# Kernel tuning notes

Measured on AMD Instinct MI355X. Metric: run time of the kernel, lower is better.

## Reference

```python
import jax, jax.numpy as jnp
import numpy as np

DIM = 512
N_HEADS = 8
HEAD_DIM = DIM // N_HEADS
BN_EPS = 1e-5


def setup_inputs() -> dict:
    key = jax.random.key(0)
    ks = jax.random.split(key, 8)
    B, C, H, W = 16, DIM, 32, 32
    x = jax.random.normal(ks[0], (B, C, H, W), dtype=jnp.float32)
    # 1x1 convs == channel matmuls: stacked q/k/v weights [3, out, in], proj [out, in]
    w_qkv = jax.random.normal(ks[1], (3, DIM, DIM), dtype=jnp.float32) * (DIM ** -0.5)
    w_proj = jax.random.normal(ks[2], (DIM, DIM), dtype=jnp.float32) * (DIM ** -0.5)
    # BatchNorm (inference form) params for q/k/v branches, stacked [3, C]
    bn_gamma = jax.random.uniform(ks[3], (3, DIM), minval=0.5, maxval=1.5)
    bn_beta = jax.random.normal(ks[4], (3, DIM)) * 0.1
    bn_mean = jax.random.normal(ks[5], (3, DIM)) * 0.1
    bn_var = jax.random.uniform(ks[6], (3, DIM), minval=0.5, maxval=1.5)
    return {"x": x, "w_qkv": w_qkv, "w_proj": w_proj, "bn_gamma": bn_gamma,
            "bn_beta": bn_beta, "bn_mean": bn_mean, "bn_var": bn_var}


def _ternary_ste(t):
    # forward: sign(t) in {-1,0,1}; backward: identity (straight-through)
    return t + jax.lax.stop_gradient(jnp.sign(t) - t)


def reference(x, w_qkv, w_proj, bn_gamma, bn_beta, bn_mean, bn_var):
    B, C, H, W = x.shape
    N = H * W
    xf = x.reshape(B, C, N)
    # fused 1x1 conv for q,k,v: [3,B,C,N]
    qkv = jnp.einsum('koc,bcn->kbon', w_qkv, xf)
    # BatchNorm (inference): y = (x - mean)/sqrt(var+eps)*gamma + beta
    s = bn_gamma / jnp.sqrt(bn_var + BN_EPS)          # [3,C]
    b = bn_beta - bn_mean * s                          # [3,C]
    qkv = qkv * s[:, None, :, None] + b[:, None, :, None]
    q = _ternary_ste(qkv[0]).reshape(B, N_HEADS, HEAD_DIM, N)
    k = _ternary_ste(qkv[1]).reshape(B, N_HEADS, HEAD_DIM, N)
    v = qkv[2].reshape(B, N_HEADS, HEAD_DIM, N)
    scale = HEAD_DIM ** -0.5
    attn = jnp.einsum('bhdn,bhen->bhde', q, k) * scale  # [B,h,d,d] channel-wise attn
    attn = jax.nn.softmax(attn, axis=-1)
    out = jnp.einsum('bhde,bhen->bhdn', attn, v).reshape(B, C, N)
    out = jnp.einsum('oc,bcn->bon', w_proj, out) + xf   # proj + residual
    return out.reshape(B, C, H, W)
```

## Files before the change

### kernel.cpp

```cpp
#include <hip/hip_runtime.h>
#include <math.h>

#define BN_EPS 1e-5f
#define FIXC 1.0e-4f

typedef _Float16 f16;
typedef _Float16 f16x4 __attribute__((ext_vector_type(4)));
typedef _Float16 f16x8 __attribute__((ext_vector_type(8)));
typedef float f32x4 __attribute__((ext_vector_type(4)));
typedef int i32x4 __attribute__((ext_vector_type(4)));

static constexpr int BB = 16;
static constexpr int C  = 512;
static constexpr int NP = 1024;
static constexpr int NH = 8;
static constexpr int HD = 64;
static constexpr int M3 = 1536;


static constexpr size_t OFF_WHI  = 0;
static constexpr size_t OFF_WLO  = 1572864;
static constexpr size_t OFF_WPH  = 3145728;
static constexpr size_t OFF_SB   = 3670016;
static constexpr size_t OFF_WN   = 3682304;
static constexpr size_t OFF_XN   = 3686400;
static constexpr size_t OFF_FLAG = 3751936;
static constexpr size_t OFF_XTH  = 5849088;
static constexpr size_t OFF_XTL  = 22626304;
static constexpr size_t OFF_AOT  = OFF_XTH;
static constexpr size_t OFF_Q    = 39403520;
static constexpr size_t OFF_K    = 47792128;
static constexpr size_t OFF_VT   = 56180736;

__device__ __forceinline__ void gld16(const void* g, void* l) {
  __builtin_amdgcn_global_load_lds(
      (const __attribute__((address_space(1))) void*)g,
      (__attribute__((address_space(3))) void*)l, 16, 0, 0);
}

__device__ __forceinline__ size_t frag_off(int tile, int kt, int row7, int k5) {
  return (((size_t)tile * 16 + kt) * 8 + (row7 >> 4)) * 512
       + (size_t)((row7 & 15) | ((k5 >> 3) << 4)) * 8;
}

__global__ __launch_bounds__(256) void k_convW(
    const float* __restrict__ wqkv, const float* __restrict__ wproj,
    const float* __restrict__ g, const float* __restrict__ be,
    const float* __restrict__ mu, const float* __restrict__ va,
    f16* __restrict__ Whi, f16* __restrict__ Wlo, f16* __restrict__ Wph,
    float* __restrict__ sA, float* __restrict__ bA)
{
  const int i = blockIdx.x * 256 + threadIdx.x;
  {
    const int m = i >> 6, l = i & 63;
    const float4 v0 = *(const float4*)&wqkv[(size_t)m * C + l * 8];
    const float4 v1 = *(const float4*)&wqkv[(size_t)m * C + l * 8 + 4];
    const float vv[8] = {v0.x, v0.y, v0.z, v0.w, v1.x, v1.y, v1.z, v1.w};
    f16x8 hv, lv;
#pragma unroll
    for (int q = 0; q < 8; ++q) {
      const f16 h = (f16)vv[q];
      hv[q] = h; lv[q] = (f16)(vv[q] - (float)h);
    }
    *(f16x8*)&Whi[frag_off(m >> 7, l >> 2, m & 127, (l & 3) * 8)] = hv;
    *(f16x8*)&Wlo[(size_t)m * C + l * 8] = lv;
  }
  if (i < 32768) {
    const int m = i >> 6, l = i & 63;
    const float4 v0 = *(const float4*)&wproj[(size_t)m * C + l * 8];
    const float4 v1 = *(const float4*)&wproj[(size_t)m * C + l * 8 + 4];
    const float vv[8] = {v0.x, v0.y, v0.z, v0.w, v1.x, v1.y, v1.z, v1.w};
    f16x8 hv;
#pragma unroll
    for (int q = 0; q < 8; ++q) hv[q] = (f16)vv[q];
    *(f16x8*)&Wph[frag_off(m >> 7, l >> 2, m & 127, (l & 3) * 8)] = hv;
  }
  if (i < M3) {
    const float s = g[i] / sqrtf(va[i] + BN_EPS);
    sA[i] = s;
    bA[i] = be[i] - mu[i] * s;
  }
}

__global__ __launch_bounds__(256) void k_wnorm(
    const float* __restrict__ wqkv, float* __restrict__ wnorm)
{
  const int row = blockIdx.x * 4 + (threadIdx.x >> 6);
  const int lane = threadIdx.x & 63;
  const float4 v0 = *(const float4*)&wqkv[(size_t)row * C + lane * 8];
  const float4 v1 = *(const float4*)&wqkv[(size_t)row * C + lane * 8 + 4];
  float s = v0.x * v0.x + v0.y * v0.y + v0.z * v0.z + v0.w * v0.w
          + v1.x * v1.x + v1.y * v1.y + v1.z * v1.z + v1.w * v1.w;
  s += __shfl_xor(s, 1);  s += __shfl_xor(s, 2);  s += __shfl_xor(s, 4);
  s += __shfl_xor(s, 8);  s += __shfl_xor(s, 16); s += __shfl_xor(s, 32);
  if (lane == 0) wnorm[row] = sqrtf(s);
}

__global__ __launch_bounds__(256) void k_convX(
    const float* __restrict__ x, f16* __restrict__ XtH, f16* __restrict__ XtL,
    float* __restrict__ xnorm2)
{
  const int k0 = blockIdx.x * 64, n0 = blockIdx.y * 64, b = blockIdx.z;
  __shared__ float ls[64][65];
  const int t = threadIdx.x;
  const float* xp = x + ((size_t)b * C + k0) * NP + n0;
  const int c4 = (t & 15) * 4, r0 = t >> 4;
#pragma unroll
  for (int q = 0; q < 4; ++q) {
    const float4 v = *(const float4*)(xp + (size_t)(r0 + q * 16) * NP + c4);
    ls[r0 + q * 16][c4 + 0] = v.x; ls[r0 + q * 16][c4 + 1] = v.y;
    ls[r0 + q * 16][c4 + 2] = v.z; ls[r0 + q * 16][c4 + 3] = v.w;
  }
  __syncthreads();
  if (t < 64) {
    float s2 = 0.f;
#pragma unroll
    for (int q = 0; q < 64; ++q) { const float v = ls[q][t]; s2 = fmaf(v, v, s2); }
    atomicAdd(&xnorm2[(b << 10) + n0 + t], s2);
  }
  const int n = t >> 2, kk = (t & 3) * 16;
  const int n_abs = n0 + n;
  f16x8 hv0 = {}, hv1 = {}, lv0 = {}, lv1 = {};
#pragma unroll
  for (int q = 0; q < 8; ++q) {
    const float v = ls[kk + q][n];
    const f16 h = (f16)v;
    hv0[q] = h; lv0[q] = (f16)(v - (float)h);
  }
#pragma unroll
  for (int q = 0; q < 8; ++q) {
    const float v = ls[kk + 8 + q][n];
    const f16 h = (f16)v;
    hv1[q] = h; lv1[q] = (f16)(v - (float)h);
  }
  const int kb0 = k0 + kk, kb1 = k0 + kk + 8;
  *(f16x8*)&XtH[frag_off(b * 8 + (n_abs >> 7), kb0 >> 5, n_abs & 127, kb0 & 31)] = hv0;
  *(f16x8*)&XtH[frag_off(b * 8 + (n_abs >> 7), kb1 >> 5, n_abs & 127, kb1 & 31)] = hv1;
  *(f16x8*)&XtL[((size_t)b * NP + n_abs) * C + kb0] = lv0;
  *(f16x8*)&XtL[((size_t)b * NP + n_abs) * C + kb1] = lv1;
}

__global__ __launch_bounds__(256) void k_qkv_mfma(
    const f16* __restrict__ Whi, const f16* __restrict__ XtH,
    const float* __restrict__ sA, const float* __restrict__ bA,
    const float* __restrict__ wnorm, const float* __restrict__ xnorm2,
    signed char* __restrict__ qw, signed char* __restrict__ kw,
    f16* __restrict__ vt, unsigned* __restrict__ flagbits)
{
  __shared__ __align__(16) f16 SMEM[32768];
  f16* const As0 = SMEM;
  f16* const Bs0 = SMEM + 8192;
  f16* const As1 = SMEM + 16384;
  f16* const Bs1 = SMEM + 24576;

  const int t = threadIdx.x, lane = t & 63, wid = t >> 6;
  const int n0 = blockIdx.x * 128, m0 = blockIdx.y * 128, b = blockIdx.z;

  const f16* Af = Whi + (size_t)(m0 >> 7) * 65536;
  const f16* Bf = XtH + ((size_t)b * 8 + (n0 >> 7)) * 65536;

  f32x4 acc[4][4];
#pragma unroll
  for (int i = 0; i < 4; ++i)
#pragma unroll
    for (int j = 0; j < 4; ++j) acc[i][j] = (f32x4){0.f, 0.f, 0.f, 0.f};

  const int wm = wid >> 1, wn = wid & 1;
  const int lr = lane & 15, ls = lane >> 4;
  const int soff = wid * 512 + lane * 8;

#define QSTAGE(TI, AS, BS) do {                                         \
    const f16* Ak_ = Af + (size_t)(TI) * 8192;                          \
    const f16* Bk_ = Bf + (size_t)(TI) * 8192;                          \
    _Pragma("unroll")                                                   \
    for (int r_ = 0; r_ < 4; ++r_) {                                    \
      gld16(Ak_ + r_ * 2048 + soff, &(AS)[r_ * 2048 + wid * 512]);      \
      gld16(Bk_ + r_ * 2048 + soff, &(BS)[r_ * 2048 + wid * 512]);      \
    }                                                                   \
  } while (0)

#define QCOMP(AS, BS) do {                                              \
    _Pragma("unroll")                                                   \
    for (int ksub_ = 0; ksub_ < 2; ++ksub_) {                           \
      f16x8 ah_[4], bh_[4];                                             \
      _Pragma("unroll")                                                 \
      for (int i_ = 0; i_ < 4; ++i_) {                                  \
        ah_[i_] = *(const f16x8*)&(AS)[ksub_ * 4096 + (wm * 4 + i_) * 512 + lane * 8]; \
        bh_[i_] = *(const f16x8*)&(BS)[ksub_ * 4096 + (wn * 4 + i_) * 512 + lane * 8]; \
      }                                                                 \
      _Pragma("unroll")                                                 \
      for (int i_ = 0; i_ < 4; ++i_)                                    \
        _Pragma("unroll")                                               \
        for (int j_ = 0; j_ < 4; ++j_)                                  \
          acc[i_][j_] = __builtin_amdgcn_mfma_f32_16x16x32_f16(         \
              ah_[i_], bh_[j_], acc[i_][j_], 0, 0, 0);                  \
    }                                                                   \
  } while (0)

  QSTAGE(0, As0, Bs0);
#pragma unroll
  for (int ti = 0; ti < 8; ++ti) {
    if (ti < 7) {
      if (ti & 1) QSTAGE(ti + 1, As0, Bs0);
      else        QSTAGE(ti + 1, As1, Bs1);
      asm volatile("s_waitcnt vmcnt(8)" ::: "memory");
    } else {
      asm volatile("s_waitcnt vmcnt(0)" ::: "memory");
    }
    __builtin_amdgcn_sched_barrier(0);
    __builtin_amdgcn_s_barrier();
    if (ti & 1) QCOMP(As1, Bs1); else QCOMP(As0, Bs0);
    asm volatile("s_waitcnt lgkmcnt(0)" ::: "memory");
    __builtin_amdgcn_sched_barrier(0);
    __builtin_amdgcn_s_barrier();
  }

#undef QSTAGE
#undef QCOMP

  const int kidx = m0 >> 9;
  if (kidx != 2) {
    signed char* dst0 = (kidx == 0) ? qw : kw;
    float xnrm[4];
#pragma unroll
    for (int j = 0; j < 4; ++j)
      xnrm[j] = sqrtf(xnorm2[(b << 10) + n0 + wn * 64 + j * 16 + lr]);
#pragma unroll
    for (int i = 0; i < 4; ++i) {
      float sv[4], bv[4], dl[4];
#pragma unroll
      for (int r = 0; r < 4; ++r) {
        const int o = m0 + wm * 64 + i * 16 + ls * 4 + r;
        sv[r] = sA[o]; bv[r] = bA[o];
        dl[r] = FIXC * wnorm[o] * sv[r];
      }
      const int oc0 = (m0 & 511) + wm * 64 + i * 16 + ls * 4;
      const int og0 = m0 + wm * 64 + i * 16 + ls * 4;
#pragma unroll
      for (int j = 0; j < 4; ++j) {
        const int n = n0 + wn * 64 + j * 16 + lr;
#pragma unroll
        for (int r = 0; r < 4; ++r) {
          const float z = fmaf(acc[i][j][r], sv[r], bv[r]);
          dst0[((size_t)b * C + oc0 + r) * NP + n] =
              (signed char)((z > 0.f) - (z < 0.f));
          if (fabsf(z) <= dl[r] * xnrm[j]) {
            const int of = og0 + r;
            atomicOr(&flagbits[(((size_t)b * NP + n) << 5) + (of >> 5)],
                     1u << (of & 31));
          }
        }
      }
    }
  } else {
    const int c0 = m0 & 511;
    for (int hf = 0; hf < 2; ++hf) {
      __syncthreads();
      if (wn == hf) {
#pragma unroll
        for (int i = 0; i < 4; ++i) {
          float sv[4], bv[4];
#pragma unroll
          for (int r = 0; r < 4; ++r) {
            const int o = m0 + wm * 64 + i * 16 + ls * 4 + r;
            sv[r] = sA[o]; bv[r] = bA[o];
          }
#pragma unroll
          for (int j = 0; j < 4; ++j) {
            f16x4 pk;
#pragma unroll
            for (int r = 0; r < 4; ++r)
              pk[r] = (f16)fmaf(acc[i][j][r], sv[r], bv[r]);
            *(f16x4*)&SMEM[(size_t)(j * 16 + lr) * 136 + wm * 64 + i * 16 + ls * 4] = pk;
          }
        }
      }
      __syncthreads();
      const int nl = t >> 2, cc = (t & 3) * 32;
      const f16* src = &SMEM[(size_t)nl * 136 + cc];
      f16x8 r0 = *(const f16x8*)(src + 0);
      f16x8 r1 = *(const f16x8*)(src + 8);
      f16x8 r2 = *(const f16x8*)(src + 16);
      f16x8 r3 = *(const f16x8*)(src + 24);
      f16* dstv = vt + ((size_t)b * NP + n0 + hf * 64 + nl) * C + c0 + cc;
      *(f16x8*)(dstv + 0)  = r0;
      *(f16x8*)(dstv + 8)  = r1;
      *(f16x8*)(dstv + 16) = r2;
      *(f16x8*)(dstv + 24) = r3;
    }
  }
}

__global__ __launch_bounds__(256) void k_fix(
    const unsigned* __restrict__ flagbits,
    const f16* __restrict__ Whi, const f16* __restrict__ Wlo,
    const f16* __restrict__ XtH, const f16* __restrict__ XtL,
    const float* __restrict__ sA, const float* __restrict__ bA,
    signed char* __restrict__ qw, signed char* __restrict__ kw)
{
  const int wv = blockIdx.x * 4 + (threadIdx.x >> 6);
  const int lane = threadIdx.x & 63;
  const int b = wv >> 10, n = wv & 1023;

  const unsigned* bm = flagbits + ((size_t)wv << 5);
  const unsigned myw = (lane < 32) ? bm[lane] : 0u;
  if (__ballot(myw != 0) == 0ULL) return;

  const int kb = lane * 8;
  const f16x8 bhv = *(const f16x8*)&XtH[
      frag_off(b * 8 + (n >> 7), kb >> 5, n & 127, kb & 31)];
  const f16x8 blv = *(const f16x8*)&XtL[((size_t)b * NP + n) * C + kb];
  float xv[8];
#pragma unroll
  for (int q = 0; q < 8; ++q) xv[q] = (float)bhv[q] + (float)blv[q];

  for (int w = 0; w < 32; ++w) {
    unsigned bits = __shfl(myw, w);
    while (bits) {
      const int o = w * 32 + __builtin_ctz(bits);
      bits &= bits - 1;
      const f16x8 ahv = *(const f16x8*)&Whi[
          frag_off(o >> 7, kb >> 5, o & 127, kb & 31)];
      const f16x8 alv = *(const f16x8*)&Wlo[(size_t)o * C + kb];
      float s = 0.f;
#pragma unroll
      for (int q = 0; q < 8; ++q)
        s = fmaf((float)ahv[q] + (float)alv[q], xv[q], s);
      s += __shfl_xor(s, 1);  s += __shfl_xor(s, 2);  s += __shfl_xor(s, 4);
      s += __shfl_xor(s, 8);  s += __shfl_xor(s, 16); s += __shfl_xor(s, 32);
      if (lane == 0) {
        const float y = fmaf(s, sA[o], bA[o]);
        const signed char sg = (signed char)((y > 0.f) - (y < 0.f));
        if (o < 512) qw[((size_t)b * C + o) * NP + n] = sg;
        else         kw[((size_t)b * C + (o - 512)) * NP + n] = sg;
      }
    }
  }
}

__global__ __launch_bounds__(256) void k_attn_fused(
    const signed char* __restrict__ qw, const signed char* __restrict__ kw,
    const f16* __restrict__ vt, f16* __restrict__ aot)
{
  const int half = blockIdx.x;
  const int bh = blockIdx.y;
  const int b = bh >> 3, h = bh & 7;
  const int t = threadIdx.x, lane = t & 63, wid = t >> 6;
  const int dw = wid * 16;
  const int lr = lane & 15, lg = lane >> 4;

  __shared__ f16 ph[64][72];
  __shared__ f16 pl[64][72];
  __shared__ f16 sb[64][72];

  const signed char* qp = qw + ((size_t)b * C + h * HD + dw + lr) * NP;
  const signed char* kp = kw + ((size_t)b * C + h * HD + lr) * NP;

  i32x4 accS[4];
#pragma unroll
  for (int j = 0; j < 4; ++j) accS[j] = (i32x4){0, 0, 0, 0};

#pragma unroll 4
  for (int ks = 0; ks < 16; ++ks) {
    const i32x4 af = *(const i32x4*)(qp + ks * 64 + lg * 16);
#pragma unroll
    for (int j = 0; j < 4; ++j) {
      const i32x4 bf = *(const i32x4*)(kp + (size_t)(j * 16) * NP + ks * 64 + lg * 16);
      accS[j] = __builtin_amdgcn_mfma_i32_16x16x64_i8(af, bf, accS[j], 0, 0, 0);
    }
  }

#pragma unroll
  for (int r = 0; r < 4; ++r) {
    float mx = (float)accS[0][r];
#pragma unroll
    for (int j = 1; j < 4; ++j) mx = fmaxf(mx, (float)accS[j][r]);
    mx = fmaxf(mx, __shfl_xor(mx, 1));
    mx = fmaxf(mx, __shfl_xor(mx, 2));
    mx = fmaxf(mx, __shfl_xor(mx, 4));
    mx = fmaxf(mx, __shfl_xor(mx, 8));
    float pvv[4];
    float sm = 0.f;
#pragma unroll
    for (int j = 0; j < 4; ++j) {
      pvv[j] = expf(((float)accS[j][r] - mx) * 0.125f);
      sm += pvv[j];
    }
    sm += __shfl_xor(sm, 1);
    sm += __shfl_xor(sm, 2);
    sm += __shfl_xor(sm, 4);
    sm += __shfl_xor(sm, 8);
    const float inv = 1.f / sm;
    const int drow = dw + lg * 4 + r;
#pragma unroll
    for (int j = 0; j < 4; ++j) {
      const float p = pvv[j] * inv;
      const f16 hi = (f16)p;
      ph[drow][j * 16 + lr] = hi;
      pl[drow][j * 16 + lr] = (f16)(p - (float)hi);
    }
  }
  __syncthreads();

  const f16x8 pa0h = *(const f16x8*)&ph[dw + lr][lg * 8];
  const f16x8 pa0l = *(const f16x8*)&pl[dw + lr][lg * 8];
  const f16x8 pa1h = *(const f16x8*)&ph[dw + lr][32 + lg * 8];
  const f16x8 pa1l = *(const f16x8*)&pl[dw + lr][32 + lg * 8];

  const f16* vbase = vt + (size_t)b * NP * C + h * HD;
  const int nbase = half * 512;

  for (int nc = 0; nc < 8; ++nc) {
    const int nn0 = nbase + nc * 64;
    __syncthreads();
#pragma unroll
    for (int nt = 0; nt < 4; ++nt) {
      const f16* vp = vbase + (size_t)(nn0 + nt * 16 + lr) * C + lg * 8;
      const f16x8 bv0 = *(const f16x8*)(vp);
      const f16x8 bv1 = *(const f16x8*)(vp + 32);
      f32x4 acc = (f32x4){0.f, 0.f, 0.f, 0.f};
      acc = __builtin_amdgcn_mfma_f32_16x16x32_f16(pa0h, bv0, acc, 0, 0, 0);
      acc = __builtin_amdgcn_mfma_f32_16x16x32_f16(pa0l, bv0, acc, 0, 0, 0);
      acc = __builtin_amdgcn_mfma_f32_16x16x32_f16(pa1h, bv1, acc, 0, 0, 0);
      acc = __builtin_amdgcn_mfma_f32_16x16x32_f16(pa1l, bv1, acc, 0, 0, 0);
      f16x4 pk;
#pragma unroll
      for (int r = 0; r < 4; ++r) pk[r] = (f16)acc[r];
      *(f16x4*)&sb[nt * 16 + lr][dw + lg * 4] = pk;
    }
    __syncthreads();
    const int nl = t >> 2, cc = (t & 3) * 16;
    const f16x8 o0 = *(const f16x8*)&sb[nl][cc];
    const f16x8 o1 = *(const f16x8*)&sb[nl][cc + 8];
    const int n_abs = nn0 + nl;
    const int c1 = h * HD + cc, c2 = h * HD + cc + 8;
    *(f16x8*)&aot[frag_off(b * 8 + (n_abs >> 7), c1 >> 5, n_abs & 127, c1 & 31)] = o0;
    *(f16x8*)&aot[frag_off(b * 8 + (n_abs >> 7), c2 >> 5, n_abs & 127, c2 & 31)] = o1;
  }
}

__global__ __launch_bounds__(256) void k_proj_mfma(
    const f16* __restrict__ Wph, const f16* __restrict__ aot,
    const float* __restrict__ X, float* __restrict__ out)
{
  __shared__ __align__(16) f16 SMEM[32768];
  f16* const As0 = SMEM;
  f16* const Bs0 = SMEM + 8192;
  f16* const As1 = SMEM + 16384;
  f16* const Bs1 = SMEM + 24576;

  const int t = threadIdx.x, lane = t & 63, wid = t >> 6;
  const int n0 = blockIdx.x * 128, m0 = blockIdx.y * 128, b = blockIdx.z;

  const f16* Af = Wph + (size_t)(m0 >> 7) * 65536;
  const f16* Bf = aot + ((size_t)b * 8 + (n0 >> 7)) * 65536;

  f32x4 acc[4][4];
#pragma unroll
  for (int i = 0; i < 4; ++i)
#pragma unroll
    for (int j = 0; j < 4; ++j) acc[i][j] = (f32x4){0.f, 0.f, 0.f, 0.f};

  const int wm = wid >> 1, wn = wid & 1;
  const int lr = lane & 15, ls = lane >> 4;
  const int soff = wid * 512 + lane * 8;

#define PSTAGE(TI, AS, BS) do {                                         \
    const f16* Ak_ = Af + (size_t)(TI) * 8192;                          \
    const f16* Bk_ = Bf + (size_t)(TI) * 8192;                          \
    _Pragma("unroll")                                                   \
    for (int r_ = 0; r_ < 4; ++r_) {                                    \
      gld16(Ak_ + r_ * 2048 + soff, &(AS)[r_ * 2048 + wid * 512]);      \
      gld16(Bk_ + r_ * 2048 + soff, &(BS)[r_ * 2048 + wid * 512]);      \
    }                                                                   \
  } while (0)

#define PCOMP(AS, BS) do {                                              \
    _Pragma("unroll")                                                   \
    for (int ksub_ = 0; ksub_ < 2; ++ksub_) {                           \
      f16x8 ah_[4], bh_[4];                                             \
      _Pragma("unroll")                                                 \
      for (int i_ = 0; i_ < 4; ++i_) {                                  \
        ah_[i_] = *(const f16x8*)&(AS)[ksub_ * 4096 + (wm * 4 + i_) * 512 + lane * 8]; \
        bh_[i_] = *(const f16x8*)&(BS)[ksub_ * 4096 + (wn * 4 + i_) * 512 + lane * 8]; \
      }                                                                 \
      _Pragma("unroll")                                                 \
      for (int i_ = 0; i_ < 4; ++i_)                                    \
        _Pragma("unroll")                                               \
        for (int j_ = 0; j_ < 4; ++j_)                                  \
          acc[i_][j_] = __builtin_amdgcn_mfma_f32_16x16x32_f16(         \
              ah_[i_], bh_[j_], acc[i_][j_], 0, 0, 0);                  \
    }                                                                   \
  } while (0)

  PSTAGE(0, As0, Bs0);
#pragma unroll
  for (int ti = 0; ti < 8; ++ti) {
    if (ti < 7) {
      if (ti & 1) PSTAGE(ti + 1, As0, Bs0);
      else        PSTAGE(ti + 1, As1, Bs1);
      asm volatile("s_waitcnt vmcnt(8)" ::: "memory");
    } else {
      asm volatile("s_waitcnt vmcnt(0)" ::: "memory");
    }
    __builtin_amdgcn_sched_barrier(0);
    __builtin_amdgcn_s_barrier();
    if (ti & 1) PCOMP(As1, Bs1); else PCOMP(As0, Bs0);
    asm volatile("s_waitcnt lgkmcnt(0)" ::: "memory");
    __builtin_amdgcn_sched_barrier(0);
    __builtin_amdgcn_s_barrier();
  }

#undef PSTAGE
#undef PCOMP

#pragma unroll
  for (int i = 0; i < 4; ++i) {
    const int oc0 = m0 + wm * 64 + i * 16 + ls * 4;
#pragma unroll
    for (int j = 0; j < 4; ++j) {
      const int n = n0 + wn * 64 + j * 16 + lr;
#pragma unroll
      for (int r = 0; r < 4; ++r) {
        const size_t idx = ((size_t)b * C + oc0 + r) * NP + n;
        out[idx] = acc[i][j][r] + X[idx];
      }
    }
  }
}

extern "C" void kernel_launch(void* const* d_in, const int* in_sizes, int n_in,
                              void* d_out, int out_size, void* d_ws, size_t ws_size,
                              hipStream_t stream)
{
  const float* x      = (const float*)d_in[0];
  const float* w_qkv  = (const float*)d_in[1];
  const float* w_proj = (const float*)d_in[2];
  const float* g      = (const float*)d_in[3];
  const float* be     = (const float*)d_in[4];
  const float* mu     = (const float*)d_in[5];
  const float* va     = (const float*)d_in[6];
  float* out = (float*)d_out;

  char* ws = (char*)d_ws;
  f16*  Whi = (f16*)(ws + OFF_WHI);
  f16*  Wlo = (f16*)(ws + OFF_WLO);
  f16*  Wph = (f16*)(ws + OFF_WPH);
  float* sA = (float*)(ws + OFF_SB);
  float* bA = sA + M3;
  float* wn = (float*)(ws + OFF_WN);
  float* xn2 = (float*)(ws + OFF_XN);
  unsigned* flagbits = (unsigned*)(ws + OFF_FLAG);
  f16*  XtH = (f16*)(ws + OFF_XTH);
  f16*  XtL = (f16*)(ws + OFF_XTL);
  f16*  aot = (f16*)(ws + OFF_AOT);
  signed char* qw = (signed char*)(ws + OFF_Q);
  signed char* kw = (signed char*)(ws + OFF_K);
  f16*  vtw = (f16*)(ws + OFF_VT);

  hipMemsetAsync(xn2, 0, OFF_XTH - OFF_XN, stream);

  k_convW<<<dim3(384), 256, 0, stream>>>(
      w_qkv, w_proj, g, be, mu, va, Whi, Wlo, Wph, sA, bA);
  k_wnorm<<<dim3(256), 256, 0, stream>>>(w_qkv, wn);
  k_convX<<<dim3(C / 64, NP / 64, BB), 256, 0, stream>>>(x, XtH, XtL, xn2);
  k_qkv_mfma<<<dim3(NP / 128, M3 / 128, BB), 256, 0, stream>>>(
      Whi, XtH, sA, bA, wn, xn2, qw, kw, vtw, flagbits);
  k_fix<<<dim3(BB * NP / 4), 256, 0, stream>>>(
      flagbits, Whi, Wlo, XtH, XtL, sA, bA, qw, kw);
  k_attn_fused<<<dim3(2, BB * NH), 256, 0, stream>>>(qw, kw, vtw, aot);
  k_proj_mfma<<<dim3(NP / 128, C / 128, BB), 256, 0, stream>>>(Wph, aot, x, out);
}
```

Measured before the change: 136.7 us.

## Fuse wnorm into convW, load QKV fragments directly to registers, split attention quarters

The separate weight-norm kernel is folded into k_convW via a wave shuffle reduction, which removes one launch. The QKV MFMA kernel drops its LDS double-buffered staging and barriers. Each wave now loads pre-fragmented operands straight from global memory into registers with a three-deep software pipeline, and shared memory shrinks so two blocks per CU can fit. The attention kernel is split into four N-chunks instead of two, doubling grid parallelism at the cost of recomputing the QK softmax in more blocks. The risk is that register-direct global loads lose the cross-wave reuse that LDS provided, since the A and B fragments are now read by two waves each.

```diff
diff --git a/kernel.cpp b/kernel.cpp
--- a/kernel.cpp
+++ b/kernel.cpp
@@ -48,7 +48,7 @@
     const float* __restrict__ g, const float* __restrict__ be,
     const float* __restrict__ mu, const float* __restrict__ va,
     f16* __restrict__ Whi, f16* __restrict__ Wlo, f16* __restrict__ Wph,
-    float* __restrict__ sA, float* __restrict__ bA)
+    float* __restrict__ sA, float* __restrict__ bA, float* __restrict__ wnorm)
 {
   const int i = blockIdx.x * 256 + threadIdx.x;
   {
@@ -57,13 +57,21 @@
     const float4 v1 = *(const float4*)&wqkv[(size_t)m * C + l * 8 + 4];
     const float vv[8] = {v0.x, v0.y, v0.z, v0.w, v1.x, v1.y, v1.z, v1.w};
     f16x8 hv, lv;
+    float s2 = 0.f;
 #pragma unroll
     for (int q = 0; q < 8; ++q) {
       const f16 h = (f16)vv[q];
       hv[q] = h; lv[q] = (f16)(vv[q] - (float)h);
+      s2 = fmaf(vv[q], vv[q], s2);
     }
     *(f16x8*)&Whi[frag_off(m >> 7, l >> 2, m & 127, (l & 3) * 8)] = hv;
     *(f16x8*)&Wlo[(size_t)m * C + l * 8] = lv;
+    if (m < 1024) {
+      s2 += __shfl_xor(s2, 1);  s2 += __shfl_xor(s2, 2);
+      s2 += __shfl_xor(s2, 4);  s2 += __shfl_xor(s2, 8);
+      s2 += __shfl_xor(s2, 16); s2 += __shfl_xor(s2, 32);
+      if (l == 0) wnorm[m] = sqrtf(s2);
+    }
   }
   if (i < 32768) {
     const int m = i >> 6, l = i & 63;
@@ -82,20 +90,6 @@
   }
 }
 
-__global__ __launch_bounds__(256) void k_wnorm(
-    const float* __restrict__ wqkv, float* __restrict__ wnorm)
-{
-  const int row = blockIdx.x * 4 + (threadIdx.x >> 6);
-  const int lane = threadIdx.x & 63;
-  const float4 v0 = *(const float4*)&wqkv[(size_t)row * C + lane * 8];
-  const float4 v1 = *(const float4*)&wqkv[(size_t)row * C + lane * 8 + 4];
-  float s = v0.x * v0.x + v0.y * v0.y + v0.z * v0.z + v0.w * v0.w
-          + v1.x * v1.x + v1.y * v1.y + v1.z * v1.z + v1.w * v1.w;
-  s += __shfl_xor(s, 1);  s += __shfl_xor(s, 2);  s += __shfl_xor(s, 4);
-  s += __shfl_xor(s, 8);  s += __shfl_xor(s, 16); s += __shfl_xor(s, 32);
-  if (lane == 0) wnorm[row] = sqrtf(s);
-}
-
 __global__ __launch_bounds__(256) void k_convX(
     const float* __restrict__ x, f16* __restrict__ XtH, f16* __restrict__ XtL,
     float* __restrict__ xnorm2)
@@ -140,18 +134,14 @@
   *(f16x8*)&XtL[((size_t)b * NP + n_abs) * C + kb1] = lv1;
 }
 
-__global__ __launch_bounds__(256) void k_qkv_mfma(
+__global__ __launch_bounds__(256, 2) void k_qkv_mfma(
     const f16* __restrict__ Whi, const f16* __restrict__ XtH,
     const float* __restrict__ sA, const float* __restrict__ bA,
     const float* __restrict__ wnorm, const float* __restrict__ xnorm2,
     signed char* __restrict__ qw, signed char* __restrict__ kw,
     f16* __restrict__ vt, unsigned* __restrict__ flagbits)
 {
-  __shared__ __align__(16) f16 SMEM[32768];
-  f16* const As0 = SMEM;
-  f16* const Bs0 = SMEM + 8192;
-  f16* const As1 = SMEM + 16384;
-  f16* const Bs1 = SMEM + 24576;
+  __shared__ __align__(16) f16 SMEM[8704];
 
   const int t = threadIdx.x, lane = t & 63, wid = t >> 6;
   const int n0 = blockIdx.x * 128, m0 = blockIdx.y * 128, b = blockIdx.z;
@@ -167,56 +157,47 @@
 
   const int wm = wid >> 1, wn = wid & 1;
   const int lr = lane & 15, ls = lane >> 4;
-  const int soff = wid * 512 + lane * 8;
-
-#define QSTAGE(TI, AS, BS) do {                                         \
-    const f16* Ak_ = Af + (size_t)(TI) * 8192;                          \
-    const f16* Bk_ = Bf + (size_t)(TI) * 8192;                          \
+
+#define LOADF(KT, AR, BR) do {                                          \
     _Pragma("unroll")                                                   \
-    for (int r_ = 0; r_ < 4; ++r_) {                                    \
-      gld16(Ak_ + r_ * 2048 + soff, &(AS)[r_ * 2048 + wid * 512]);      \
-      gld16(Bk_ + r_ * 2048 + soff, &(BS)[r_ * 2048 + wid * 512]);      \
+    for (int i_ = 0; i_ < 4; ++i_) {                                    \
+      (AR)[i_] = *(const f16x8*)&Af[(size_t)(KT) * 4096 + (wm * 4 + i_) * 512 + lane * 8]; \
+      (BR)[i_] = *(const f16x8*)&Bf[(size_t)(KT) * 4096 + (wn * 4 + i_) * 512 + lane * 8]; \
     }                                                                   \
   } while (0)
 
-#define QCOMP(AS, BS) do {                                              \
+#define COMPF(AR, BR) do {                                              \
     _Pragma("unroll")                                                   \
-    for (int ksub_ = 0; ksub_ < 2; ++ksub_) {                           \
-      f16x8 ah_[4], bh_[4];                                             \
+    for (int i_ = 0; i_ < 4; ++i_)                                      \
       _Pragma("unroll")                                                 \
-      for (int i_ = 0; i_ < 4; ++i_) {                                  \
-        ah_[i_] = *(const f16x8*)&(AS)[ksub_ * 4096 + (wm * 4 + i_) * 512 + lane * 8]; \
-        bh_[i_] = *(const f16x8*)&(BS)[ksub_ * 4096 + (wn * 4 + i_) * 512 + lane * 8]; \
-      }                                                                 \
-      _Pragma("unroll")                                                 \
-      for (int i_ = 0; i_ < 4; ++i_)                                    \
-        _Pragma("unroll")                                               \
-        for (int j_ = 0; j_ < 4; ++j_)                                  \
-          acc[i_][j_] = __builtin_amdgcn_mfma_f32_16x16x32_f16(         \
-              ah_[i_], bh_[j_], acc[i_][j_], 0, 0, 0);                  \
-    }                                                                   \
+      for (int j_ = 0; j_ < 4; ++j_)                                    \
+        acc[i_][j_] = __builtin_amdgcn_mfma_f32_16x16x32_f16(           \
+            (AR)[i_], (BR)[j_], acc[i_][j_], 0, 0, 0);                  \
   } while (0)
 
-  QSTAGE(0, As0, Bs0);
-#pragma unroll
-  for (int ti = 0; ti < 8; ++ti) {
-    if (ti < 7) {
-      if (ti & 1) QSTAGE(ti + 1, As0, Bs0);
-      else        QSTAGE(ti + 1, As1, Bs1);
-      asm volatile("s_waitcnt vmcnt(8)" ::: "memory");
-    } else {
-      asm volatile("s_waitcnt vmcnt(0)" ::: "memory");
-    }
-    __builtin_amdgcn_sched_barrier(0);
-    __builtin_amdgcn_s_barrier();
-    if (ti & 1) QCOMP(As1, Bs1); else QCOMP(As0, Bs0);
-    asm volatile("s_waitcnt lgkmcnt(0)" ::: "memory");
-    __builtin_amdgcn_sched_barrier(0);
-    __builtin_amdgcn_s_barrier();
-  }
-
-#undef QSTAGE
-#undef QCOMP
+  {
+    f16x8 a0[4], b0[4], a1[4], b1[4], a2[4], b2[4];
+    LOADF(0, a0, b0); LOADF(1, a1, b1);
+    LOADF(2,  a2, b2); COMPF(a0, b0);
+    LOADF(3,  a0, b0); COMPF(a1, b1);
+    LOADF(4,  a1, b1); COMPF(a2, b2);
+    LOADF(5,  a2, b2); COMPF(a0, b0);
+    LOADF(6,  a0, b0); COMPF(a1, b1);
+    LOADF(7,  a1, b1); COMPF(a2, b2);
+    LOADF(8,  a2, b2); COMPF(a0, b0);
+    LOADF(9,  a0, b0); COMPF(a1, b1);
+    LOADF(10, a1, b1); COMPF(a2, b2);
+    LOADF(11, a2, b2); COMPF(a0, b0);
+    LOADF(12, a0, b0); COMPF(a1, b1);
+    LOADF(13, a1, b1); COMPF(a2, b2);
+    LOADF(14, a2, b2); COMPF(a0, b0);
+    LOADF(15, a0, b0); COMPF(a1, b1);
+    COMPF(a2, b2);
+    COMPF(a0, b0);
+  }
+
+#undef LOADF
+#undef COMPF
 
   const int kidx = m0 >> 9;
   if (kidx != 2) {
@@ -342,7 +323,7 @@
     const signed char* __restrict__ qw, const signed char* __restrict__ kw,
     const f16* __restrict__ vt, f16* __restrict__ aot)
 {
-  const int half = blockIdx.x;
+  const int quarter = blockIdx.x;
   const int bh = blockIdx.y;
   const int b = bh >> 3, h = bh & 7;
   const int t = threadIdx.x, lane = t & 63, wid = t >> 6;
@@ -408,9 +389,9 @@
   const f16x8 pa1l = *(const f16x8*)&pl[dw + lr][32 + lg * 8];
 
   const f16* vbase = vt + (size_t)b * NP * C + h * HD;
-  const int nbase = half * 512;
-
-  for (int nc = 0; nc < 8; ++nc) {
+  const int nbase = quarter * 256;
+
+  for (int nc = 0; nc < 4; ++nc) {
     const int nn0 = nbase + nc * 64;
     __syncthreads();
 #pragma unroll
@@ -561,13 +542,12 @@
   hipMemsetAsync(xn2, 0, OFF_XTH - OFF_XN, stream);
 
   k_convW<<<dim3(384), 256, 0, stream>>>(
-      w_qkv, w_proj, g, be, mu, va, Whi, Wlo, Wph, sA, bA);
-  k_wnorm<<<dim3(256), 256, 0, stream>>>(w_qkv, wn);
+      w_qkv, w_proj, g, be, mu, va, Whi, Wlo, Wph, sA, bA, wn);
   k_convX<<<dim3(C / 64, NP / 64, BB), 256, 0, stream>>>(x, XtH, XtL, xn2);
   k_qkv_mfma<<<dim3(NP / 128, M3 / 128, BB), 256, 0, stream>>>(
       Whi, XtH, sA, bA, wn, xn2, qw, kw, vtw, flagbits);
   k_fix<<<dim3(BB * NP / 4), 256, 0, stream>>>(
       flagbits, Whi, Wlo, XtH, XtL, sA, bA, qw, kw);
-  k_attn_fused<<<dim3(2, BB * NH), 256, 0, stream>>>(qw, kw, vtw, aot);
+  k_attn_fused<<<dim3(4, BB * NH), 256, 0, stream>>>(qw, kw, vtw, aot);
   k_proj_mfma<<<dim3(NP / 128, C / 128, BB), 256, 0, stream>>>(Wph, aot, x, out);
 }
```

After: 142.6 us. 4.3% more time.
